# Performance work log

Measured on AMD Instinct MI355X. Metric: run time of the kernel, lower is better.

The kernel has to match this reference:

```python
import jax, jax.numpy as jnp
import numpy as np

NEG_INF = -1e30  # stand-in for -inf in additive causal mask (softmax-safe)


def rotary_pos_emb(x):
    # x: [B, T, H, D]. Faithful to source: freqs = 1/1000**(arange(0,D,2)//D)
    # with INTEGER floor division -> exponent 0 -> all freqs == 1.0.
    B, T, H, D = x.shape
    exponents = (jnp.arange(0, D, 2)[: D // 2] // D).astype(jnp.float32)
    freqs = 1.0 / jnp.power(jnp.float32(1000.0), exponents)          # [D/2]
    theta = jnp.arange(T, dtype=jnp.float32)[:, None] * freqs[None, :]  # [T, D/2]
    cos = jnp.cos(theta)[None, :, None, :]  # [1, T, 1, D/2]
    sin = jnp.sin(theta)[None, :, None, :]
    xr = x.astype(jnp.float32).reshape(B, T, H, D // 2, 2)
    x0, x1 = xr[..., 0], xr[..., 1]
    # complex multiply (x0 + i x1) * (cos + i sin)
    out = jnp.stack([x0 * cos - x1 * sin, x0 * sin + x1 * cos], axis=-1)
    return out.reshape(B, T, H, D).astype(x.dtype)


def attention_fwd(x, wq, wk, wv, wo, n_heads=32):
    B, T, C = x.shape
    hd = C // n_heads  # head_dim = 128
    # nn.Linear(bias=False): y = x @ W^T with W: [out, in]
    xq = (x @ wq.T).reshape(B, T, n_heads, hd)
    xk = (x @ wk.T).reshape(B, T, n_heads, hd)
    xv = (x @ wv.T).reshape(B, T, n_heads, hd)
    xq = rotary_pos_emb(xq)
    xk = rotary_pos_emb(xk)
    # n_rep == 1 -> repeat_kv is identity
    scale = hd ** -0.5
    scores = jnp.einsum('bqhd,bkhd->bhqk', xq, xk) * scale  # [B,H,T,T]
    causal = jnp.tril(jnp.ones((T, T), dtype=bool))
    scores = jnp.where(causal[None, None], scores, NEG_INF)
    probs = jax.nn.softmax(scores.astype(jnp.float32), axis=-1).astype(xq.dtype)
    out = jnp.einsum('bhqk,bkhd->bqhd', probs, xv).reshape(B, T, C)
    return out @ wo.T


def setup_inputs() -> dict:
    key = jax.random.key(0)
    ks = jax.random.split(key, 5)
    B, T, C = 2, 2048, 4096
    s = 0.02
    return {
        'x': jax.random.normal(ks[0], (B, T, C), jnp.float32),
        'wq': jax.random.normal(ks[1], (C, C), jnp.float32) * s,
        'wk': jax.random.normal(ks[2], (C, C), jnp.float32) * s,
        'wv': jax.random.normal(ks[3], (C, C), jnp.float32) * s,
        'wo': jax.random.normal(ks[4], (C, C), jnp.float32) * s,
    }


def reference(x, wq, wk, wv, wo):
    return attention_fwd(x, wq, wk, wv, wo)
```

## Files before the change

kernel.cpp:

```cpp
#include <hip/hip_runtime.h>
#include <hip/hip_bf16.h>
#include <stdint.h>

typedef __bf16 bf16_t;
typedef __attribute__((ext_vector_type(8))) __bf16 bf16x8;
typedef __attribute__((ext_vector_type(4))) float f32x4;

#define GLL16(gptr, lptr)                                                      \
  __builtin_amdgcn_global_load_lds(                                            \
      (__attribute__((address_space(1))) void*)(gptr),                         \
      (__attribute__((address_space(3))) void*)(lptr), 16, 0, 0)

__global__ __launch_bounds__(256) void cast5_kernel(const float* __restrict__ x,
                                                    const float* __restrict__ wq,
                                                    const float* __restrict__ wk,
                                                    const float* __restrict__ wv,
                                                    const float* __restrict__ wo,
                                                    bf16_t* __restrict__ outbase) {
  const size_t SZ = (size_t)4096 * 4096;
  const float* in;
  switch (blockIdx.y) {
    case 0: in = x; break;
    case 1: in = wq; break;
    case 2: in = wk; break;
    case 3: in = wv; break;
    default: in = wo; break;
  }
  bf16_t* out = outbase + (size_t)blockIdx.y * SZ;
  int i = blockIdx.x * 256 + threadIdx.x;
  const float4* p = (const float4*)in + (size_t)i * 2;
  float4 a = p[0], b = p[1];
  bf16x8 o;
  o[0] = (__bf16)a.x; o[1] = (__bf16)a.y; o[2] = (__bf16)a.z; o[3] = (__bf16)a.w;
  o[4] = (__bf16)b.x; o[5] = (__bf16)b.y; o[6] = (__bf16)b.z; o[7] = (__bf16)b.w;
  *((bf16x8*)out + i) = o;
}

#define STAGE_HALF(gbase, ldsbase)                                             \
  do {                                                                         \
    GLL16((gbase) + (size_t)(w * 32 + sr) * 4096 + sq, (ldsbase) + w * 1024);  \
    GLL16((gbase) + (size_t)(w * 32 + 16 + sr) * 4096 + sq,                    \
          (ldsbase) + w * 1024 + 512);                                         \
  } while (0)

#define PHASE(mh_, kk_, buf_, LOADB_, STAGE_STMT, TAIL_STMT)                   \
  do {                                                                         \
    bf16x8 af_[4];                                                             \
    _Pragma("unroll") for (int mi = 0; mi < 4; ++mi) af_[mi] =                 \
        *(const bf16x8*)&As[buf_][kk_][(wr * 128 + (mh_)*64 + mi * 16 + l15) * \
                                           32 +                                \
                                       sl8];                                   \
    if (LOADB_) {                                                              \
      _Pragma("unroll") for (int ni = 0; ni < 4; ++ni) bfr[ni] =               \
          *(const bf16x8*)&Bs[buf_][kk_][(wc * 64 + ni * 16 + l15) * 32 +      \
                                         sl8];                                 \
    }                                                                          \
    STAGE_STMT;                                                                \
    __builtin_amdgcn_s_barrier();                                              \
    asm volatile("s_waitcnt lgkmcnt(0)" ::: "memory");                         \
    __builtin_amdgcn_sched_barrier(0);                                         \
    __builtin_amdgcn_s_setprio(1);                                             \
    _Pragma("unroll") for (int mi = 0; mi < 4; ++mi)                           \
        _Pragma("unroll") for (int ni = 0; ni < 4; ++ni)                       \
            acc[(mh_)*4 + mi][ni] = __builtin_amdgcn_mfma_f32_16x16x32_bf16(   \
                af_[mi], bfr[ni], acc[(mh_)*4 + mi][ni], 0, 0, 0);             \
    __builtin_amdgcn_s_setprio(0);                                             \
    __builtin_amdgcn_sched_barrier(0);                                         \
    TAIL_STMT;                                                                 \
    __builtin_amdgcn_s_barrier();                                              \
  } while (0)

#define GEMM256_MAIN(Aptr, Bptr)                                               \
  const bf16_t* Ag = (Aptr) + (size_t)bm * 4096;                               \
  const bf16_t* Bg = (Bptr) + (size_t)bn * 4096;                               \
  f32x4 acc[8][4] = {};                                                        \
  bf16x8 bfr[4];                                                               \
  STAGE_HALF(Ag, &As[0][0][0]);                                                \
  STAGE_HALF(Bg, &Bs[0][0][0]);                                                \
  STAGE_HALF(Ag + 32, &As[0][1][0]);                                           \
  STAGE_HALF(Bg + 32, &Bs[0][1][0]);                                           \
  STAGE_HALF(Ag + 64, &As[1][0][0]);                                           \
  STAGE_HALF(Bg + 64, &Bs[1][0][0]);                                           \
  asm volatile("s_waitcnt vmcnt(4)" ::: "memory");                             \
  __builtin_amdgcn_s_barrier();                                                \
  for (int it = 0; it < 32; ++it) {                                            \
    const int kt = it * 2;                                                     \
    const bool more = (it < 31);                                               \
    PHASE(0, 0, 0, 1,                                                          \
          STAGE_HALF(Ag + (size_t)(kt + 1) * 64 + 32, &As[1][1][0]), (void)0); \
    PHASE(1, 0, 0, 0,                                                          \
          STAGE_HALF(Bg + (size_t)(kt + 1) * 64 + 32, &Bs[1][1][0]), (void)0); \
    PHASE(0, 1, 0, 1,                                                          \
          if (more) STAGE_HALF(Ag + (size_t)(kt + 2) * 64, &As[0][0][0]),      \
          (void)0);                                                            \
    PHASE(1, 1, 0, 0,                                                          \
          if (more) STAGE_HALF(Bg + (size_t)(kt + 2) * 64, &Bs[0][0][0]),      \
          if (more) { asm volatile("s_waitcnt vmcnt(4)" ::: "memory"); } else {\
            asm volatile("s_waitcnt vmcnt(0)" ::: "memory"); });               \
    PHASE(0, 0, 1, 1,                                                          \
          if (more) STAGE_HALF(Ag + (size_t)(kt + 2) * 64 + 32, &As[0][1][0]), \
          (void)0);                                                            \
    PHASE(1, 0, 1, 0,                                                          \
          if (more) STAGE_HALF(Bg + (size_t)(kt + 2) * 64 + 32, &Bs[0][1][0]), \
          (void)0);                                                            \
    PHASE(0, 1, 1, 1,                                                          \
          if (more) STAGE_HALF(Ag + (size_t)(kt + 3) * 64, &As[1][0][0]),      \
          (void)0);                                                            \
    PHASE(1, 1, 1, 0,                                                          \
          if (more) STAGE_HALF(Bg + (size_t)(kt + 3) * 64, &Bs[1][0][0]),      \
          if (more) { asm volatile("s_waitcnt vmcnt(4)" ::: "memory"); } else {\
            asm volatile("s_waitcnt vmcnt(0)" ::: "memory"); });               \
  }

__device__ __forceinline__ void epi_rope256(const f32x4 (&acc)[8][4],
                                            bf16_t* __restrict__ C, int bm,
                                            int bn, int wr, int wc, int quad,
                                            int l15) {
#pragma unroll
  for (int a = 0; a < 8; ++a) {
    const int row0 = bm + wr * 128 + a * 16 + quad * 4;
    float fsv[4], fcv[4];
#pragma unroll
    for (int r = 0; r < 4; ++r)
      sincosf((float)((row0 + r) & 2047), &fsv[r], &fcv[r]);
#pragma unroll
    for (int ni = 0; ni < 4; ++ni) {
      const int col = bn + wc * 64 + ni * 16 + l15;
      const bool odd = (col & 1);
#pragma unroll
      for (int r = 0; r < 4; ++r) {
        float v = acc[a][ni][r];
        float pr = __shfl_xor(v, 1, 64);
        float o = odd ? (pr * fsv[r] + v * fcv[r]) : (v * fcv[r] - pr * fsv[r]);
        C[(size_t)(row0 + r) * 4096 + col] = (__bf16)o;
      }
    }
  }
}

__device__ __forceinline__ void epi_vt256(const f32x4 (&acc)[8][4],
                                          bf16_t* __restrict__ VT, int bm,
                                          int bn, int wr, int wc, int quad,
                                          int l15) {
#pragma unroll
  for (int a = 0; a < 8; ++a) {
    const int row0 = bm + wr * 128 + a * 16 + quad * 4;
    const int b = row0 >> 11, t0 = row0 & 2047;
#pragma unroll
    for (int ni = 0; ni < 4; ++ni) {
      const int col = bn + wc * 64 + ni * 16 + l15;
      const int h = col >> 7, d = col & 127;
      union { __bf16 e[4]; uint2 u; } pk;
#pragma unroll
      for (int r = 0; r < 4; ++r) pk.e[r] = (__bf16)acc[a][ni][r];
      *(uint2*)&VT[((size_t)((b * 32 + h) * 128 + d)) * 2048 + t0] = pk.u;
    }
  }
}

__global__ __launch_bounds__(512, 2) void gemm_qkv(const bf16_t* __restrict__ X,
                                                   const bf16_t* __restrict__ WQ,
                                                   const bf16_t* __restrict__ WK,
                                                   const bf16_t* __restrict__ WV,
                                                   bf16_t* __restrict__ Qo,
                                                   bf16_t* __restrict__ Ko,
                                                   bf16_t* __restrict__ VTo) {
  __shared__ bf16_t As[2][2][8192];
  __shared__ bf16_t Bs[2][2][8192];
  const int tid = threadIdx.x;
  const int w = tid >> 6;
  const int lane = tid & 63;
  const int quad = lane >> 4;
  const int l15 = lane & 15;
  const int wr = w >> 2, wc = w & 3;
  const int sr = lane >> 2;
  const int sq = (((lane & 3) ^ ((lane >> 3) & 3))) * 8;
  const int sl8 = (quad ^ ((l15 >> 1) & 3)) * 8;
  const int mat = blockIdx.y;
  int id = blockIdx.x;
  id = (id & 7) * 32 + (id >> 3);
  const int bm = (id >> 4) * 256, bn = (id & 15) * 256;
  const bf16_t* Bp = (mat == 0) ? WQ : (mat == 1) ? WK : WV;

  GEMM256_MAIN(X, Bp)

  if (mat == 0)
    epi_rope256(acc, Qo, bm, bn, wr, wc, quad, l15);
  else if (mat == 1)
    epi_rope256(acc, Ko, bm, bn, wr, wc, quad, l15);
  else
    epi_vt256(acc, VTo, bm, bn, wr, wc, quad, l15);
}

__global__ __launch_bounds__(512, 2) void gemm_out(const bf16_t* __restrict__ A,
                                                   const bf16_t* __restrict__ B,
                                                   float* __restrict__ C) {
  __shared__ bf16_t As[2][2][8192];
  __shared__ bf16_t Bs[2][2][8192];
  const int tid = threadIdx.x;
  const int w = tid >> 6;
  const int lane = tid & 63;
  const int quad = lane >> 4;
  const int l15 = lane & 15;
  const int wr = w >> 2, wc = w & 3;
  const int sr = lane >> 2;
  const int sq = (((lane & 3) ^ ((lane >> 3) & 3))) * 8;
  const int sl8 = (quad ^ ((l15 >> 1) & 3)) * 8;
  int id = blockIdx.x;
  id = (id & 7) * 32 + (id >> 3);
  const int bm = (id >> 4) * 256, bn = (id & 15) * 256;

  GEMM256_MAIN(A, B)

#pragma unroll
  for (int a = 0; a < 8; ++a) {
    const int row0 = bm + wr * 128 + a * 16 + quad * 4;
#pragma unroll
    for (int ni = 0; ni < 4; ++ni) {
      const int col = bn + wc * 64 + ni * 16 + l15;
#pragma unroll
      for (int r = 0; r < 4; ++r)
        C[(size_t)(row0 + r) * 4096 + col] = acc[a][ni][r];
    }
  }
}

__global__ __launch_bounds__(256) void attn_kernel(const bf16_t* __restrict__ Q,
                                                   const bf16_t* __restrict__ Km,
                                                   const bf16_t* __restrict__ VT,
                                                   bf16_t* __restrict__ O) {
  __shared__ bf16_t Ks[64 * 128];
  __shared__ bf16_t Vts[128 * 64];
  __shared__ bf16_t QPs[64 * 128];
  const int tid = threadIdx.x;
  const int w = tid >> 6;
  const int lane = tid & 63;
  const int quad = lane >> 4;
  const int l15 = lane & 15;
  const int bh = blockIdx.x;
  const int qtile = 31 - blockIdx.y;
  const int mrow_base = (bh >> 5) * 2048;
  const int h = bh & 31;
  const float scale = 0.08838834764831845f;

#pragma unroll
  for (int it = 0; it < 4; ++it) {
    int c = w * 4 + it;
    int row = c * 4 + (lane >> 4);
    int cc = (lane & 15) ^ (row & 15);
    GLL16(Q + (size_t)(mrow_base + qtile * 64 + row) * 4096 + h * 128 + cc * 8,
          &QPs[c * 512]);
  }
  __syncthreads();
  bf16x8 qf[4];
#pragma unroll
  for (int ks = 0; ks < 4; ++ks) {
    int row = w * 16 + l15;
    int slot = (ks * 4 + quad) ^ (row & 15);
    qf[ks] = *(const bf16x8*)&QPs[row * 128 + slot * 8];
  }
  bf16_t* Pw = &QPs[w * 16 * 72];

  f32x4 accO[8] = {};
  float mrun[4], lrun[4];
#pragma unroll
  for (int r = 0; r < 4; ++r) { mrun[r] = -1e30f; lrun[r] = 0.f; }

  for (int kt = 0; kt <= qtile; ++kt) {
    __syncthreads();
#pragma unroll
    for (int it = 0; it < 4; ++it) {
      int c = w * 4 + it;
      int krow = c * 4 + (lane >> 4);
      int kcc = (lane & 15) ^ (krow & 15);
      GLL16(Km + (size_t)(mrow_base + kt * 64 + krow) * 4096 + h * 128 + kcc * 8,
            &Ks[c * 512]);
      int vrow = c * 8 + (lane >> 3);
      int vcc = (lane & 7) ^ (vrow & 7);
      GLL16(VT + (size_t)(bh * 128 + vrow) * 2048 + kt * 64 + vcc * 8,
            &Vts[c * 512]);
    }
    __syncthreads();

    f32x4 s[4];
#pragma unroll
    for (int ni = 0; ni < 4; ++ni) {
      s[ni] = (f32x4){0.f, 0.f, 0.f, 0.f};
#pragma unroll
      for (int ks = 0; ks < 4; ++ks) {
        int row = ni * 16 + l15;
        int slot = (ks * 4 + quad) ^ (row & 15);
        bf16x8 kf = *(const bf16x8*)&Ks[row * 128 + slot * 8];
        s[ni] = __builtin_amdgcn_mfma_f32_16x16x32_bf16(qf[ks], kf, s[ni], 0, 0, 0);
      }
    }
    const bool diag = (kt == qtile);
#pragma unroll
    for (int ni = 0; ni < 4; ++ni)
#pragma unroll
      for (int r = 0; r < 4; ++r) {
        float v = s[ni][r] * scale;
        if (diag && (ni * 16 + l15) > (w * 16 + quad * 4 + r)) v = -1e30f;
        s[ni][r] = v;
      }
    float mx[4], alpha[4], rs[4];
#pragma unroll
    for (int r = 0; r < 4; ++r)
      mx[r] = fmaxf(fmaxf(s[0][r], s[1][r]), fmaxf(s[2][r], s[3][r]));
#pragma unroll
    for (int off = 1; off < 16; off <<= 1)
#pragma unroll
      for (int r = 0; r < 4; ++r) mx[r] = fmaxf(mx[r], __shfl_xor(mx[r], off, 64));
    float ps[4][4];
#pragma unroll
    for (int r = 0; r < 4; ++r) {
      float mn = fmaxf(mrun[r], mx[r]);
      alpha[r] = __expf(mrun[r] - mn);
      mrun[r] = mn;
      rs[r] = 0.f;
    }
#pragma unroll
    for (int ni = 0; ni < 4; ++ni)
#pragma unroll
      for (int r = 0; r < 4; ++r) {
        float p = __expf(s[ni][r] - mrun[r]);
        ps[ni][r] = p;
        rs[r] += p;
      }
#pragma unroll
    for (int off = 1; off < 16; off <<= 1)
#pragma unroll
      for (int r = 0; r < 4; ++r) rs[r] += __shfl_xor(rs[r], off, 64);
#pragma unroll
    for (int r = 0; r < 4; ++r) lrun[r] = lrun[r] * alpha[r] + rs[r];
#pragma unroll
    for (int nt = 0; nt < 8; ++nt)
#pragma unroll
      for (int r = 0; r < 4; ++r) accO[nt][r] *= alpha[r];
#pragma unroll
    for (int ni = 0; ni < 4; ++ni)
#pragma unroll
      for (int r = 0; r < 4; ++r)
        Pw[(quad * 4 + r) * 72 + ni * 16 + l15] = (__bf16)ps[ni][r];
    asm volatile("s_waitcnt lgkmcnt(0)" ::: "memory");
    bf16x8 pf[2];
#pragma unroll
    for (int ks = 0; ks < 2; ++ks)
      pf[ks] = *(const bf16x8*)&Pw[l15 * 72 + ks * 32 + quad * 8];
#pragma unroll
    for (int nt = 0; nt < 8; ++nt)
#pragma unroll
      for (int ks = 0; ks < 2; ++ks) {
        int vrow = nt * 16 + l15;
        int slot = (ks * 4 + quad) ^ (vrow & 7);
        bf16x8 vf = *(const bf16x8*)&Vts[vrow * 64 + slot * 8];
        accO[nt] = __builtin_amdgcn_mfma_f32_16x16x32_bf16(pf[ks], vf, accO[nt], 0, 0, 0);
      }
  }

#pragma unroll
  for (int r = 0; r < 4; ++r) lrun[r] = 1.f / lrun[r];
#pragma unroll
  for (int nt = 0; nt < 8; ++nt)
#pragma unroll
    for (int r = 0; r < 4; ++r) {
      int trow = qtile * 64 + w * 16 + quad * 4 + r;
      int d = nt * 16 + l15;
      O[(size_t)(mrow_base + trow) * 4096 + h * 128 + d] =
          (__bf16)(accO[nt][r] * lrun[r]);
    }
}

extern "C" void kernel_launch(void* const* d_in, const int* in_sizes, int n_in,
                              void* d_out, int out_size, void* d_ws, size_t ws_size,
                              hipStream_t stream) {
  (void)in_sizes; (void)n_in; (void)out_size; (void)ws_size;
  const float* x = (const float*)d_in[0];
  const float* wq = (const float*)d_in[1];
  const float* wk = (const float*)d_in[2];
  const float* wv = (const float*)d_in[3];
  const float* wo = (const float*)d_in[4];
  float* out = (float*)d_out;

  const size_t SZ = (size_t)4096 * 4096;
  bf16_t* xb = (bf16_t*)d_ws;
  bf16_t* wqb = xb + SZ;
  bf16_t* wkb = wqb + SZ;
  bf16_t* wvb = wkb + SZ;
  bf16_t* wob = wvb + SZ;
  bf16_t* qb = wob + SZ;
  bf16_t* kb = qb + SZ;
  bf16_t* vtb = kb + SZ;
  bf16_t* ab = vtb + SZ;

  dim3 b256(256), b512(512);
  cast5_kernel<<<dim3((unsigned)(SZ / 8 / 256), 5), b256, 0, stream>>>(
      x, wq, wk, wv, wo, xb);

  gemm_qkv<<<dim3(256, 3), b512, 0, stream>>>(xb, wqb, wkb, wvb, qb, kb, vtb);

  attn_kernel<<<dim3(64, 32), b256, 0, stream>>>(qb, kb, vtb, ab);

  gemm_out<<<dim3(256), b512, 0, stream>>>(ab, wob, out);
}
```

Measured before the change: 1.049 ms.

## Merge GEMM phase pairs to halve barriers and overlap LDS reads with MFMA

Each pair of PHASE steps in the bf16 GEMM main loop becomes one HALF step. The step loads the B fragments and the first A fragments, issues the A staging, then reads the second A fragments while the first 16 MFMAs run, using a partial lgkmcnt wait. This halves the workgroup barriers per K-step and hides LDS read latency behind matrix work. In exchange it needs more registers for two live A fragment sets, and the reordered waits and barriers make the synchronisation more fragile.

```diff
diff --git a/kernel.cpp b/kernel.cpp
--- a/kernel.cpp
+++ b/kernel.cpp
@@ -43,30 +43,36 @@
           (ldsbase) + w * 1024 + 512);                                         \
   } while (0)
 
-#define PHASE(mh_, kk_, buf_, LOADB_, STAGE_STMT, TAIL_STMT)                   \
+#define HALF(buf_, kk_, S1_, S2_, TAIL_)                                       \
   do {                                                                         \
-    bf16x8 af_[4];                                                             \
-    _Pragma("unroll") for (int mi = 0; mi < 4; ++mi) af_[mi] =                 \
-        *(const bf16x8*)&As[buf_][kk_][(wr * 128 + (mh_)*64 + mi * 16 + l15) * \
-                                           32 +                                \
+    bf16x8 af0_[4], af1_[4];                                                   \
+    _Pragma("unroll") for (int ni = 0; ni < 4; ++ni) bfr[ni] =                 \
+        *(const bf16x8*)&Bs[buf_][kk_][(wc * 64 + ni * 16 + l15) * 32 + sl8];  \
+    _Pragma("unroll") for (int mi = 0; mi < 4; ++mi) af0_[mi] =                \
+        *(const bf16x8*)&As[buf_][kk_][(wr * 128 + mi * 16 + l15) * 32 + sl8]; \
+    S1_;                                                                       \
+    __builtin_amdgcn_sched_barrier(0);                                         \
+    _Pragma("unroll") for (int mi = 0; mi < 4; ++mi) af1_[mi] =                \
+        *(const bf16x8*)&As[buf_][kk_][(wr * 128 + 64 + mi * 16 + l15) * 32 +  \
                                        sl8];                                   \
-    if (LOADB_) {                                                              \
-      _Pragma("unroll") for (int ni = 0; ni < 4; ++ni) bfr[ni] =               \
-          *(const bf16x8*)&Bs[buf_][kk_][(wc * 64 + ni * 16 + l15) * 32 +      \
-                                         sl8];                                 \
-    }                                                                          \
-    STAGE_STMT;                                                                \
-    __builtin_amdgcn_s_barrier();                                              \
+    asm volatile("s_waitcnt lgkmcnt(4)" ::: "memory");                         \
+    __builtin_amdgcn_sched_barrier(0);                                         \
+    __builtin_amdgcn_s_setprio(1);                                             \
+    _Pragma("unroll") for (int mi = 0; mi < 4; ++mi)                           \
+        _Pragma("unroll") for (int ni = 0; ni < 4; ++ni)                       \
+            acc[mi][ni] = __builtin_amdgcn_mfma_f32_16x16x32_bf16(             \
+                af0_[mi], bfr[ni], acc[mi][ni], 0, 0, 0);                      \
+    __builtin_amdgcn_s_setprio(0);                                             \
+    S2_;                                                                       \
     asm volatile("s_waitcnt lgkmcnt(0)" ::: "memory");                         \
     __builtin_amdgcn_sched_barrier(0);                                         \
     __builtin_amdgcn_s_setprio(1);                                             \
     _Pragma("unroll") for (int mi = 0; mi < 4; ++mi)                           \
         _Pragma("unroll") for (int ni = 0; ni < 4; ++ni)                       \
-            acc[(mh_)*4 + mi][ni] = __builtin_amdgcn_mfma_f32_16x16x32_bf16(   \
-                af_[mi], bfr[ni], acc[(mh_)*4 + mi][ni], 0, 0, 0);             \
+            acc[4 + mi][ni] = __builtin_amdgcn_mfma_f32_16x16x32_bf16(         \
+                af1_[mi], bfr[ni], acc[4 + mi][ni], 0, 0, 0);                  \
     __builtin_amdgcn_s_setprio(0);                                             \
-    __builtin_amdgcn_sched_barrier(0);                                         \
-    TAIL_STMT;                                                                 \
+    TAIL_;                                                                     \
     __builtin_amdgcn_s_barrier();                                              \
   } while (0)
 
@@ -86,30 +92,24 @@
   for (int it = 0; it < 32; ++it) {                                            \
     const int kt = it * 2;                                                     \
     const bool more = (it < 31);                                               \
-    PHASE(0, 0, 0, 1,                                                          \
-          STAGE_HALF(Ag + (size_t)(kt + 1) * 64 + 32, &As[1][1][0]), (void)0); \
-    PHASE(1, 0, 0, 0,                                                          \
-          STAGE_HALF(Bg + (size_t)(kt + 1) * 64 + 32, &Bs[1][1][0]), (void)0); \
-    PHASE(0, 1, 0, 1,                                                          \
-          if (more) STAGE_HALF(Ag + (size_t)(kt + 2) * 64, &As[0][0][0]),      \
-          (void)0);                                                            \
-    PHASE(1, 1, 0, 0,                                                          \
-          if (more) STAGE_HALF(Bg + (size_t)(kt + 2) * 64, &Bs[0][0][0]),      \
-          if (more) { asm volatile("s_waitcnt vmcnt(4)" ::: "memory"); } else {\
-            asm volatile("s_waitcnt vmcnt(0)" ::: "memory"); });               \
-    PHASE(0, 0, 1, 1,                                                          \
-          if (more) STAGE_HALF(Ag + (size_t)(kt + 2) * 64 + 32, &As[0][1][0]), \
-          (void)0);                                                            \
-    PHASE(1, 0, 1, 0,                                                          \
-          if (more) STAGE_HALF(Bg + (size_t)(kt + 2) * 64 + 32, &Bs[0][1][0]), \
-          (void)0);                                                            \
-    PHASE(0, 1, 1, 1,                                                          \
-          if (more) STAGE_HALF(Ag + (size_t)(kt + 3) * 64, &As[1][0][0]),      \
-          (void)0);                                                            \
-    PHASE(1, 1, 1, 0,                                                          \
-          if (more) STAGE_HALF(Bg + (size_t)(kt + 3) * 64, &Bs[1][0][0]),      \
-          if (more) { asm volatile("s_waitcnt vmcnt(4)" ::: "memory"); } else {\
-            asm volatile("s_waitcnt vmcnt(0)" ::: "memory"); });               \
+                                                    \
+    HALF(0, 0,                                                                 \
+         STAGE_HALF(Ag + (size_t)(kt + 1) * 64 + 32, &As[1][1][0]),            \
+         STAGE_HALF(Bg + (size_t)(kt + 1) * 64 + 32, &Bs[1][1][0]), (void)0);  \
+    HALF(0, 1,                                                                 \
+         if (more) STAGE_HALF(Ag + (size_t)(kt + 2) * 64, &As[0][0][0]),       \
+         if (more) STAGE_HALF(Bg + (size_t)(kt + 2) * 64, &Bs[0][0][0]),       \
+         if (more) { asm volatile("s_waitcnt vmcnt(4)" ::: "memory"); } else { \
+           asm volatile("s_waitcnt vmcnt(0)" ::: "memory"); });                \
+                                                  \
+    HALF(1, 0,                                                                 \
+         if (more) STAGE_HALF(Ag + (size_t)(kt + 2) * 64 + 32, &As[0][1][0]),  \
+         if (more) STAGE_HALF(Bg + (size_t)(kt + 2) * 64 + 32, &Bs[0][1][0]),  \
+         (void)0);                                                             \
+    HALF(1, 1,                                                                 \
+         if (more) STAGE_HALF(Ag + (size_t)(kt + 3) * 64, &As[1][0][0]),       \
+         if (more) STAGE_HALF(Bg + (size_t)(kt + 3) * 64, &Bs[1][0][0]),       \
+         if (more) { asm volatile("s_waitcnt vmcnt(4)" ::: "memory"); });      \
   }
 
 __device__ __forceinline__ void epi_rope256(const f32x4 (&acc)[8][4],
```

Measured after the change: 1.009 ms. 1.04x faster.

## Restructure GEMM main loop into register-prefetched two-buffer K pipeline

Applied to the files above, without the earlier changes.

Replaces the 8-phase, 4-slot LDS pipeline of the 256x256 GEMMs with a 2-slot LDS ring. LDS fragments for the next k-step are prefetched into registers while the current MFMA clusters run, so each k-step has two barriers instead of one per phase. This halves LDS use and cuts barrier count, which may permit higher occupancy. In exchange the global prefetch distance is shorter and register pressure grows from the extra fragment buffers. The epilogue row mapping is updated to match the new accumulator order.

```diff
diff --git a/kernel.cpp b/kernel.cpp
--- a/kernel.cpp
+++ b/kernel.cpp
@@ -43,73 +43,58 @@
           (ldsbase) + w * 1024 + 512);                                         \
   } while (0)
 
-#define PHASE(mh_, kk_, buf_, LOADB_, STAGE_STMT, TAIL_STMT)                   \
+#define MFMA_CL(ACCB_, AF_, BF_)                                               \
+  __builtin_amdgcn_sched_barrier(0);                                           \
+  __builtin_amdgcn_s_setprio(1);                                               \
+  _Pragma("unroll") for (int mi = 0; mi < 4; ++mi)                             \
+      _Pragma("unroll") for (int ni = 0; ni < 4; ++ni)                         \
+          acc[(ACCB_) + mi][ni] = __builtin_amdgcn_mfma_f32_16x16x32_bf16(     \
+              AF_[mi], BF_[ni], acc[(ACCB_) + mi][ni], 0, 0, 0);               \
+  __builtin_amdgcn_s_setprio(0);
+
+#define KITER(P_, AF0C_, BFC_, AF0N_, BFN_, KT_, MORE_)                        \
   do {                                                                         \
-    bf16x8 af_[4];                                                             \
-    _Pragma("unroll") for (int mi = 0; mi < 4; ++mi) af_[mi] =                 \
-        *(const bf16x8*)&As[buf_][kk_][(wr * 128 + (mh_)*64 + mi * 16 + l15) * \
-                                           32 +                                \
-                                       sl8];                                   \
-    if (LOADB_) {                                                              \
-      _Pragma("unroll") for (int ni = 0; ni < 4; ++ni) bfr[ni] =               \
-          *(const bf16x8*)&Bs[buf_][kk_][(wc * 64 + ni * 16 + l15) * 32 +      \
-                                         sl8];                                 \
-    }                                                                          \
-    STAGE_STMT;                                                                \
-    __builtin_amdgcn_s_barrier();                                              \
+    _Pragma("unroll") for (int mi = 0; mi < 4; ++mi) af1t[mi] =                \
+        *(const bf16x8*)&As[P_][(wr * 128 + 64 + mi * 16 + l15) * 32 + sl8];   \
+    MFMA_CL(0, AF0C_, BFC_)                                                    \
     asm volatile("s_waitcnt lgkmcnt(0)" ::: "memory");                         \
     __builtin_amdgcn_sched_barrier(0);                                         \
-    __builtin_amdgcn_s_setprio(1);                                             \
-    _Pragma("unroll") for (int mi = 0; mi < 4; ++mi)                           \
-        _Pragma("unroll") for (int ni = 0; ni < 4; ++ni)                       \
-            acc[(mh_)*4 + mi][ni] = __builtin_amdgcn_mfma_f32_16x16x32_bf16(   \
-                af_[mi], bfr[ni], acc[(mh_)*4 + mi][ni], 0, 0, 0);             \
-    __builtin_amdgcn_s_setprio(0);                                             \
-    __builtin_amdgcn_sched_barrier(0);                                         \
-    TAIL_STMT;                                                                 \
-    __builtin_amdgcn_s_barrier();                                              \
+    __builtin_amdgcn_s_barrier();    \
+    if (MORE_) {                                                               \
+      STAGE_HALF(Ag + (size_t)(KT_ + 2) * 32, &As[P_][0]);                     \
+      STAGE_HALF(Bg + (size_t)(KT_ + 2) * 32, &Bs[P_][0]);                     \
+      asm volatile("s_waitcnt vmcnt(4)" ::: "memory");                         \
+    } else {                                                                   \
+      asm volatile("s_waitcnt vmcnt(0)" ::: "memory");                         \
+    }                                                                          \
+    __builtin_amdgcn_s_barrier();                \
+    _Pragma("unroll") for (int ni = 0; ni < 4; ++ni) BFN_[ni] =                \
+        *(const bf16x8*)&Bs[P_ ^ 1][(wc * 64 + ni * 16 + l15) * 32 + sl8];     \
+    _Pragma("unroll") for (int mi = 0; mi < 4; ++mi) AF0N_[mi] =               \
+        *(const bf16x8*)&As[P_ ^ 1][(wr * 128 + mi * 16 + l15) * 32 + sl8];    \
+    MFMA_CL(4, af1t, BFC_)                                                     \
   } while (0)
 
 #define GEMM256_MAIN(Aptr, Bptr)                                               \
   const bf16_t* Ag = (Aptr) + (size_t)bm * 4096;                               \
   const bf16_t* Bg = (Bptr) + (size_t)bn * 4096;                               \
   f32x4 acc[8][4] = {};                                                        \
-  bf16x8 bfr[4];                                                               \
-  STAGE_HALF(Ag, &As[0][0][0]);                                                \
-  STAGE_HALF(Bg, &Bs[0][0][0]);                                                \
-  STAGE_HALF(Ag + 32, &As[0][1][0]);                                           \
-  STAGE_HALF(Bg + 32, &Bs[0][1][0]);                                           \
-  STAGE_HALF(Ag + 64, &As[1][0][0]);                                           \
-  STAGE_HALF(Bg + 64, &Bs[1][0][0]);                                           \
-  asm volatile("s_waitcnt vmcnt(4)" ::: "memory");                             \
+  bf16x8 af0A[4], af0B[4], bfA[4], bfB[4], af1t[4];                            \
+  STAGE_HALF(Ag, &As[0][0]);                                                   \
+  STAGE_HALF(Bg, &Bs[0][0]);                                                   \
+  STAGE_HALF(Ag + 32, &As[1][0]);                                              \
+  STAGE_HALF(Bg + 32, &Bs[1][0]);                                              \
+  asm volatile("s_waitcnt vmcnt(4)" ::: "memory");           \
   __builtin_amdgcn_s_barrier();                                                \
-  for (int it = 0; it < 32; ++it) {                                            \
-    const int kt = it * 2;                                                     \
-    const bool more = (it < 31);                                               \
-    PHASE(0, 0, 0, 1,                                                          \
-          STAGE_HALF(Ag + (size_t)(kt + 1) * 64 + 32, &As[1][1][0]), (void)0); \
-    PHASE(1, 0, 0, 0,                                                          \
-          STAGE_HALF(Bg + (size_t)(kt + 1) * 64 + 32, &Bs[1][1][0]), (void)0); \
-    PHASE(0, 1, 0, 1,                                                          \
-          if (more) STAGE_HALF(Ag + (size_t)(kt + 2) * 64, &As[0][0][0]),      \
-          (void)0);                                                            \
-    PHASE(1, 1, 0, 0,                                                          \
-          if (more) STAGE_HALF(Bg + (size_t)(kt + 2) * 64, &Bs[0][0][0]),      \
-          if (more) { asm volatile("s_waitcnt vmcnt(4)" ::: "memory"); } else {\
-            asm volatile("s_waitcnt vmcnt(0)" ::: "memory"); });               \
-    PHASE(0, 0, 1, 1,                                                          \
-          if (more) STAGE_HALF(Ag + (size_t)(kt + 2) * 64 + 32, &As[0][1][0]), \
-          (void)0);                                                            \
-    PHASE(1, 0, 1, 0,                                                          \
-          if (more) STAGE_HALF(Bg + (size_t)(kt + 2) * 64 + 32, &Bs[0][1][0]), \
-          (void)0);                                                            \
-    PHASE(0, 1, 1, 1,                                                          \
-          if (more) STAGE_HALF(Ag + (size_t)(kt + 3) * 64, &As[1][0][0]),      \
-          (void)0);                                                            \
-    PHASE(1, 1, 1, 0,                                                          \
-          if (more) STAGE_HALF(Bg + (size_t)(kt + 3) * 64, &Bs[1][0][0]),      \
-          if (more) { asm volatile("s_waitcnt vmcnt(4)" ::: "memory"); } else {\
-            asm volatile("s_waitcnt vmcnt(0)" ::: "memory"); });               \
+  _Pragma("unroll") for (int ni = 0; ni < 4; ++ni) bfA[ni] =                   \
+      *(const bf16x8*)&Bs[0][(wc * 64 + ni * 16 + l15) * 32 + sl8];            \
+  _Pragma("unroll") for (int mi = 0; mi < 4; ++mi) af0A[mi] =                  \
+      *(const bf16x8*)&As[0][(wr * 128 + mi * 16 + l15) * 32 + sl8];           \
+  for (int jj = 0; jj < 64; ++jj) {                                            \
+    const int kt = jj * 2;                                                     \
+    const bool m = (jj < 63);                                                  \
+    KITER(0, af0A, bfA, af0B, bfB, kt, m);                                     \
+    KITER(1, af0B, bfB, af0A, bfA, kt + 1, m);                                 \
   }
 
 __device__ __forceinline__ void epi_rope256(const f32x4 (&acc)[8][4],
@@ -118,7 +103,7 @@
                                             int l15) {
 #pragma unroll
   for (int a = 0; a < 8; ++a) {
-    const int row0 = bm + wr * 128 + a * 16 + quad * 4;
+    const int row0 = bm + wr * 128 + (a & 3) * 16 + (a >> 2) * 64 + quad * 4;
     float fsv[4], fcv[4];
 #pragma unroll
     for (int r = 0; r < 4; ++r)
@@ -144,7 +129,7 @@
                                           int l15) {
 #pragma unroll
   for (int a = 0; a < 8; ++a) {
-    const int row0 = bm + wr * 128 + a * 16 + quad * 4;
+    const int row0 = bm + wr * 128 + (a & 3) * 16 + (a >> 2) * 64 + quad * 4;
     const int b = row0 >> 11, t0 = row0 & 2047;
 #pragma unroll
     for (int ni = 0; ni < 4; ++ni) {
@@ -165,8 +150,8 @@
                                                    bf16_t* __restrict__ Qo,
                                                    bf16_t* __restrict__ Ko,
                                                    bf16_t* __restrict__ VTo) {
-  __shared__ bf16_t As[2][2][8192];
-  __shared__ bf16_t Bs[2][2][8192];
+  __shared__ bf16_t As[2][8192];
+  __shared__ bf16_t Bs[2][8192];
   const int tid = threadIdx.x;
   const int w = tid >> 6;
   const int lane = tid & 63;
@@ -195,8 +180,8 @@
 __global__ __launch_bounds__(512, 2) void gemm_out(const bf16_t* __restrict__ A,
                                                    const bf16_t* __restrict__ B,
                                                    float* __restrict__ C) {
-  __shared__ bf16_t As[2][2][8192];
-  __shared__ bf16_t Bs[2][2][8192];
+  __shared__ bf16_t As[2][8192];
+  __shared__ bf16_t Bs[2][8192];
   const int tid = threadIdx.x;
   const int w = tid >> 6;
   const int lane = tid & 63;
@@ -214,7 +199,7 @@
 
 #pragma unroll
   for (int a = 0; a < 8; ++a) {
-    const int row0 = bm + wr * 128 + a * 16 + quad * 4;
+    const int row0 = bm + wr * 128 + (a & 3) * 16 + (a >> 2) * 64 + quad * 4;
 #pragma unroll
     for (int ni = 0; ni < 4; ++ni) {
       const int col = bn + wc * 64 + ni * 16 + l15;
```

After: 1.117 ms. 6.5% more time.
